# Performance work log

Measured on AMD Instinct MI355X. Metric: run time of the kernel, lower is better.

## Reference

```python
import jax, jax.numpy as jnp
import numpy as np

N, E, D, H = 50000, 800000, 64, 64  # nodes, edges, feat dim, hidden dim
EPS = 1e-3  # Keras BatchNormalization default epsilon

def bn(x, g, b, mu, v):
    # inference-mode batch norm with moving statistics
    return (x - mu) * jax.lax.rsqrt(v + EPS) * g + b

def gelu(x):
    return jax.nn.gelu(x, approximate=False)  # tf.nn.gelu default is exact

def setup_inputs() -> dict:
    key = jax.random.key(0)
    ks = jax.random.split(key, 24)
    r = lambda i, shape, s=1.0: (jax.random.normal(ks[i], shape, jnp.float32) * s)
    inp = {
        "node_feats": r(0, (N, D)),
        "edge_feats": r(1, (E, D)),
        "src": jax.random.randint(ks[2], (E,), 0, N, jnp.int32),
        "dst": jax.random.randint(ks[3], (E,), 0, N, jnp.int32),
        # message MLP (BN -> Dense(gelu)) x2, input D
        "m_g1": 1.0 + 0.1 * r(4, (D,)), "m_b1": 0.1 * r(5, (D,)),
        "m_mu1": 0.1 * r(6, (D,)), "m_v1": jnp.ones((D,), jnp.float32),
        "m_W1": r(7, (D, H), 1.0 / np.sqrt(D)), "m_c1": jnp.zeros((H,), jnp.float32),
        "m_g2": 1.0 + 0.1 * r(8, (H,)), "m_b2": 0.1 * r(9, (H,)),
        "m_mu2": 0.1 * r(10, (H,)), "m_v2": jnp.ones((H,), jnp.float32),
        "m_W2": r(11, (H, H), 1.0 / np.sqrt(H)), "m_c2": jnp.zeros((H,), jnp.float32),
        # edge transformer MLP (Dense(gelu)) x2, input D
        "e_W1": r(12, (D, H), 1.0 / np.sqrt(D)), "e_c1": jnp.zeros((H,), jnp.float32),
        "e_W2": r(13, (H, H), 1.0 / np.sqrt(H)), "e_c2": jnp.zeros((H,), jnp.float32),
        # update MLP (BN -> Dense(gelu)) x2, input D+H (concat combination)
        "u_g1": 1.0 + 0.1 * r(14, (D + H,)), "u_b1": 0.1 * r(15, (D + H,)),
        "u_mu1": 0.1 * r(16, (D + H,)), "u_v1": jnp.ones((D + H,), jnp.float32),
        "u_W1": r(17, (D + H, H), 1.0 / np.sqrt(D + H)), "u_c1": jnp.zeros((H,), jnp.float32),
        "u_g2": 1.0 + 0.1 * r(18, (H,)), "u_b2": 0.1 * r(19, (H,)),
        "u_mu2": 0.1 * r(20, (H,)), "u_v2": jnp.ones((H,), jnp.float32),
        "u_W2": r(21, (H, H), 1.0 / np.sqrt(H)), "u_c2": jnp.zeros((H,), jnp.float32),
    }
    return inp

def reference(node_feats, edge_feats,
              m_g1, m_b1, m_mu1, m_v1, m_W1, m_c1,
              m_g2, m_b2, m_mu2, m_v2, m_W2, m_c2,
              e_W1, e_c1, e_W2, e_c2,
              u_g1, u_b1, u_mu1, u_v1, u_W1, u_c1,
              u_g2, u_b2, u_mu2, u_v2, u_W2, u_c2,
              src, dst):
    # gather neighbour representations: [E, D]
    nbr = node_feats[dst]
    # base message MLP: (BN -> Dropout(identity at inference) -> Dense gelu) x2
    h = gelu(bn(nbr, m_g1, m_b1, m_mu1, m_v1) @ m_W1 + m_c1)
    msg = gelu(bn(h, m_g2, m_b2, m_mu2, m_v2) @ m_W2 + m_c2)
    # edge transformer: Dense(gelu) x2, gates the messages elementwise
    er = gelu(edge_feats @ e_W1 + e_c1)
    er = gelu(er @ e_W2 + e_c2)
    msg = msg * er  # [E, H]
    # unsorted_segment_mean over source node indices (empty segments -> 0)
    s = jax.ops.segment_sum(msg, src, num_segments=N)
    cnt = jax.ops.segment_sum(jnp.ones((E, 1), msg.dtype), src, num_segments=N)
    agg = s / jnp.maximum(cnt, 1.0)  # [N, H]
    # combine ('concat') and update MLP
    hcat = jnp.concatenate([node_feats, agg], axis=-1)  # [N, D+H]
    h = gelu(bn(hcat, u_g1, u_b1, u_mu1, u_v1) @ u_W1 + u_c1)
    out = gelu(bn(h, u_g2, u_b2, u_mu2, u_v2) @ u_W2 + u_c2)
    return out  # [N, H]
```

## Files before the change

kernel.cpp:

```cpp
#include <hip/hip_runtime.h>
#include <hip/hip_bf16.h>

#define NN 50000
#define NE 800000

typedef __bf16 bf16_t;
typedef bf16_t bf16x8 __attribute__((ext_vector_type(8)));
typedef float f32x4 __attribute__((ext_vector_type(4)));

__device__ __forceinline__ float gelu_f(float x) {
    float v = x * fmaf(x * x, 0.07135481627f, 1.595769122f);
    float e = __expf(-v);
    return x * __builtin_amdgcn_rcpf(1.0f + e);
}

__device__ void fold_frag(int K, const float* W, const float* g, const float* b,
                          const float* mu, const float* v, const float* c,
                          bf16_t* Wf, float* cb, int tid, float* part) {
    const int n = tid & 63, kc = tid >> 6;
    const int nt = n >> 4, lrow = n & 15, nkc = K >> 5;
    const int kq = K >> 2, k0 = kc * kq, k1 = k0 + kq;
    float acc = 0.f;
    for (int k = k0; k < k1; ++k) {
        float w = W[k * 64 + n];
        float s = 1.0f, o = 0.0f;
        if (g) {
            s = g[k] * __frsqrt_rn(v[k] + 1e-3f);
            o = b[k] - mu[k] * s;
        }
        int idx = ((nt * nkc + (k >> 5)) * 64 + ((k >> 3) & 3) * 16 + lrow) * 8 + (k & 7);
        Wf[idx] = (bf16_t)(w * s);
        acc += o * w;
    }
    part[kc * 64 + n] = acc;
    __syncthreads();
    if (kc == 0) cb[n] = c[n] + part[n] + part[64 + n] + part[128 + n] + part[192 + n];
}

__global__ void fold_kernel(
    const float* mg1, const float* mb1, const float* mmu1, const float* mv1,
    const float* mW1, const float* mc1,
    const float* mg2, const float* mb2, const float* mmu2, const float* mv2,
    const float* mW2, const float* mc2,
    const float* eW1, const float* ec1, const float* eW2, const float* ec2,
    const float* ug1, const float* ub1, const float* umu1, const float* uv1,
    const float* uW1, const float* uc1,
    const float* ug2, const float* ub2, const float* umu2, const float* uv2,
    const float* uW2, const float* uc2,
    bf16_t* wcat, bf16_t* uW1f, bf16_t* uW2f,
    float* cm1, float* cm2, float* ce1, float* ce2, float* cu1, float* cu2)
{
    __shared__ float part[256];
    int t = threadIdx.x;
    switch (blockIdx.x) {
        case 0: fold_frag(64,  mW1, mg1, mb1, mmu1, mv1, mc1, wcat,         cm1, t, part); break;
        case 1: fold_frag(64,  mW2, mg2, mb2, mmu2, mv2, mc2, wcat + 4096,  cm2, t, part); break;
        case 2: fold_frag(64,  eW1, nullptr, nullptr, nullptr, nullptr, ec1, wcat + 8192,  ce1, t, part); break;
        case 3: fold_frag(64,  eW2, nullptr, nullptr, nullptr, nullptr, ec2, wcat + 12288, ce2, t, part); break;
        case 4: fold_frag(128, uW1, ug1, ub1, umu1, uv1, uc1, uW1f, cu1, t, part); break;
        case 5: fold_frag(64,  uW2, ug2, ub2, umu2, uv2, uc2, uW2f, cu2, t, part); break;
    }
}

__global__ void hist_kernel(const int* __restrict__ src, int* __restrict__ cnt) {
    int e = blockIdx.x * 256 + threadIdx.x;
    if (e < NE) atomicAdd(&cnt[src[e]], 1);
}

__global__ void scanA_kernel(const int* __restrict__ cnt, int* __restrict__ part,
                             int* __restrict__ btot) {
    __shared__ int s[256];
    int tid = threadIdx.x;
    int i = blockIdx.x * 256 + tid;
    int v = (i < NN) ? cnt[i] : 0;
    s[tid] = v;
    __syncthreads();
    #pragma unroll
    for (int off = 1; off < 256; off <<= 1) {
        int t = (tid >= off) ? s[tid - off] : 0;
        __syncthreads();
        s[tid] += t;
        __syncthreads();
    }
    if (i < NN) part[i] = s[tid] - v;
    if (tid == 255) btot[blockIdx.x] = s[255];
}

__global__ void scanB_kernel(int* __restrict__ btot, int nblk) {
    __shared__ int s[256];
    int tid = threadIdx.x;
    int v = (tid < nblk) ? btot[tid] : 0;
    s[tid] = v;
    __syncthreads();
    #pragma unroll
    for (int off = 1; off < 256; off <<= 1) {
        int t = (tid >= off) ? s[tid - off] : 0;
        __syncthreads();
        s[tid] += t;
        __syncthreads();
    }
    if (tid < nblk) btot[tid] = s[tid] - v;
}

__global__ void scanC_kernel(const int* __restrict__ part, const int* __restrict__ btot,
                             int* __restrict__ woff) {
    int i = blockIdx.x * 256 + threadIdx.x;
    if (i < NN) woff[i] = part[i] + btot[i >> 8];
}

__device__ __forceinline__ void mk_frag_hilo(const float* row, int quad,
        bf16x8& hi0, bf16x8& lo0, bf16x8& hi1, bf16x8& lo1)
{
    #pragma unroll
    for (int j = 0; j < 8; ++j) {
        float x0 = row[quad * 8 + j];
        float x1 = row[32 + quad * 8 + j];
        bf16_t h0 = (bf16_t)x0, h1 = (bf16_t)x1;
        hi0[j] = h0; lo0[j] = (bf16_t)(x0 - (float)h0);
        hi1[j] = h1; lo1[j] = (bf16_t)(x1 - (float)h1);
    }
}

__device__ __forceinline__ bf16x8 ldb(const bf16_t* wf, int slot, int lane) {
    return *(const bf16x8*)(wf + (slot * 64 + lane) * 8);
}

__device__ __forceinline__ void gemm64_hilo(const bf16_t* wf, int m,
        bf16x8 h0, bf16x8 l0, bf16x8 h1, bf16x8 l1, f32x4 (&acc)[4], int lane)
{
    #pragma unroll
    for (int nt = 0; nt < 4; ++nt) {
        bf16x8 b0 = ldb(wf, m * 8 + nt * 2 + 0, lane);
        bf16x8 b1 = ldb(wf, m * 8 + nt * 2 + 1, lane);
        f32x4 c = {0.f, 0.f, 0.f, 0.f};
        c = __builtin_amdgcn_mfma_f32_16x16x32_bf16(h0, b0, c, 0, 0, 0);
        c = __builtin_amdgcn_mfma_f32_16x16x32_bf16(l0, b0, c, 0, 0, 0);
        c = __builtin_amdgcn_mfma_f32_16x16x32_bf16(h1, b1, c, 0, 0, 0);
        c = __builtin_amdgcn_mfma_f32_16x16x32_bf16(l1, b1, c, 0, 0, 0);
        acc[nt] = c;
    }
}

__device__ __forceinline__ void gemm64(const bf16_t* wf, int m,
        bf16x8 a0, bf16x8 a1, f32x4 (&acc)[4], int lane)
{
    #pragma unroll
    for (int nt = 0; nt < 4; ++nt) {
        bf16x8 b0 = ldb(wf, m * 8 + nt * 2 + 0, lane);
        bf16x8 b1 = ldb(wf, m * 8 + nt * 2 + 1, lane);
        f32x4 c = {0.f, 0.f, 0.f, 0.f};
        c = __builtin_amdgcn_mfma_f32_16x16x32_bf16(a0, b0, c, 0, 0, 0);
        c = __builtin_amdgcn_mfma_f32_16x16x32_bf16(a1, b1, c, 0, 0, 0);
        acc[nt] = c;
    }
}

__device__ __forceinline__ void epi_to_frag(const f32x4 (&acc)[4], const float* bias,
        bf16_t* h, int lrow, int quad)
{
    #pragma unroll
    for (int nt = 0; nt < 4; ++nt) {
        float bb = bias[nt * 16 + lrow];
        #pragma unroll
        for (int r = 0; r < 4; ++r)
            h[((nt * 2 + (lrow >> 3)) * 16 + quad * 4 + r) * 8 + (lrow & 7)] =
                (bf16_t)gelu_f(acc[nt][r] + bb);
    }
}

__global__ __launch_bounds__(256) void node_msg_kernel(
    const float* __restrict__ node_feats, const bf16_t* __restrict__ wcat,
    const float* __restrict__ cm1, const float* __restrict__ cm2,
    bf16_t* __restrict__ msg)
{
    __shared__ bf16_t wf[8192];
    __shared__ bf16_t hf[4][1024];

    const int tid  = threadIdx.x;
    const int wave = tid >> 6;
    const int lane = tid & 63;
    const int quad = lane >> 4;
    const int lrow = lane & 15;

    #pragma unroll
    for (int i = 0; i < 4; ++i) {
        int chunk = tid + i * 256;
        *(bf16x8*)(wf + chunk * 8) = *(const bf16x8*)(wcat + chunk * 8);
    }
    __syncthreads();

    const int nbase = blockIdx.x * 64 + wave * 16;
    int arow = nbase + lrow;
    arow = arow < NN ? arow : NN - 1;

    f32x4 acc[4];
    {
        const float* nrow = node_feats + (size_t)arow * 64;
        bf16x8 h0, l0, h1, l1;
        mk_frag_hilo(nrow, quad, h0, l0, h1, l1);
        gemm64_hilo(wf, 0, h0, l0, h1, l1, acc, lane);
        epi_to_frag(acc, cm1, hf[wave], lrow, quad);
    }
    bf16x8 a0 = *(const bf16x8*)(hf[wave] + lane * 8);
    bf16x8 a1 = *(const bf16x8*)(hf[wave] + (lane + 64) * 8);
    gemm64(wf, 1, a0, a1, acc, lane);

    #pragma unroll
    for (int nt = 0; nt < 4; ++nt) {
        float bb = cm2[nt * 16 + lrow];
        #pragma unroll
        for (int r = 0; r < 4; ++r) {
            int row = nbase + quad * 4 + r;
            if (row < NN)
                msg[(size_t)row * 64 + nt * 16 + lrow] = (bf16_t)gelu_f(acc[nt][r] + bb);
        }
    }
}

__global__ __launch_bounds__(256) void edge_kernel(
    const float* __restrict__ edge_feats,
    const int* __restrict__ src, const int* __restrict__ dst,
    const bf16_t* __restrict__ wcat,
    const float* __restrict__ ce1, const float* __restrict__ ce2,
    const bf16_t* __restrict__ msg,
    float* __restrict__ s_acc, int* __restrict__ woff,
    bf16_t* __restrict__ buf, int use_csr)
{
    __shared__ bf16_t wf[8192];
    __shared__ bf16_t hf[4][1024];

    const int tid  = threadIdx.x;
    const int wave = tid >> 6;
    const int lane = tid & 63;
    const int quad = lane >> 4;
    const int lrow = lane & 15;

    #pragma unroll
    for (int i = 0; i < 4; ++i) {
        int chunk = tid + i * 256;
        *(bf16x8*)(wf + chunk * 8) = *(const bf16x8*)(wcat + 8192 + chunk * 8);
    }
    __syncthreads();

    const int ebase = blockIdx.x * 64 + wave * 16;
    bf16_t* h = hf[wave];
    const int r0 = lane >> 3;
    const int c0 = lane & 7;
    const int r1 = 8 + r0;
    const int b0 = r0 * 64 + ((c0 * 8) ^ (((r0 >> 2) & 3) << 4));
    const int b1 = r1 * 64 + ((c0 * 8) ^ (((r1 >> 2) & 3) << 4));

    int dA = dst[ebase + r0];
    int dB = dst[ebase + r1];
    bf16x8 mA = *(const bf16x8*)(msg + (size_t)dA * 64 + c0 * 8);
    bf16x8 mB = *(const bf16x8*)(msg + (size_t)dB * 64 + c0 * 8);
    int pe_l = 0;
    if (use_csr && lane < 16) pe_l = atomicAdd(&woff[src[ebase + lane]], 1);

    f32x4 acc[4];
    {
        const float* efr = edge_feats + (size_t)(ebase + lrow) * 64;
        bf16x8 h0_, l0_, h1_, l1_;
        mk_frag_hilo(efr, quad, h0_, l0_, h1_, l1_);
        gemm64_hilo(wf, 0, h0_, l0_, h1_, l1_, acc, lane);
        epi_to_frag(acc, ce1, h, lrow, quad);
    }
    bf16x8 a0 = *(const bf16x8*)(h + lane * 8);
    bf16x8 a1 = *(const bf16x8*)(h + (lane + 64) * 8);
    __builtin_amdgcn_wave_barrier();
    *(bf16x8*)(h + b0) = mA;
    *(bf16x8*)(h + b1) = mB;
    __builtin_amdgcn_wave_barrier();

    gemm64(wf, 1, a0, a1, acc, lane);
    __builtin_amdgcn_wave_barrier();

    if (use_csr) {
        #pragma unroll
        for (int nt = 0; nt < 4; ++nt) {
            float bb = ce2[nt * 16 + lrow];
            #pragma unroll
            for (int r = 0; r < 4; ++r) {
                int e = quad * 4 + r;
                int ci = e * 64 + ((nt * 16 + lrow) ^ (((e >> 2) & 3) << 4));
                float er = gelu_f(acc[nt][r] + bb);
                h[ci] = (bf16_t)(er * (float)h[ci]);
            }
        }
        __builtin_amdgcn_wave_barrier();
        int peA = __shfl(pe_l, r0);
        int peB = __shfl(pe_l, r1);
        bf16x8 gA = *(const bf16x8*)(h + b0);
        bf16x8 gB = *(const bf16x8*)(h + b1);
        *(bf16x8*)(buf + (size_t)peA * 64 + c0 * 8) = gA;
        *(bf16x8*)(buf + (size_t)peB * 64 + c0 * 8) = gB;
    } else {
        #pragma unroll
        for (int nt = 0; nt < 4; ++nt) {
            float bb = ce2[nt * 16 + lrow];
            #pragma unroll
            for (int r = 0; r < 4; ++r) {
                int e = quad * 4 + r;
                int ci = e * 64 + ((nt * 16 + lrow) ^ (((e >> 2) & 3) << 4));
                float er = gelu_f(acc[nt][r] + bb);
                unsafeAtomicAdd(&s_acc[(size_t)src[ebase + e] * 64 + nt * 16 + lrow],
                                er * (float)h[ci]);
            }
        }
    }
}

__global__ __launch_bounds__(256) void agg_kernel(
    const bf16_t* __restrict__ buf, const int* __restrict__ woff,
    const int* __restrict__ cnt, float* __restrict__ agg)
{
    const int wave = threadIdx.x >> 6;
    const int lane = threadIdx.x & 63;
    const int n = blockIdx.x * 4 + wave;
    const int deg = cnt[n];
    const int end = woff[n];
    const int start = end - deg;
    const int rg = lane >> 3;
    const int cc = lane & 7;

    float a[8] = {0.f, 0.f, 0.f, 0.f, 0.f, 0.f, 0.f, 0.f};
    for (int b = start; b < end; b += 8) {
        int row = b + rg;
        if (row < end) {
            bf16x8 v = *(const bf16x8*)(buf + (size_t)row * 64 + cc * 8);
            #pragma unroll
            for (int j = 0; j < 8; ++j) a[j] += (float)v[j];
        }
    }
    #pragma unroll
    for (int off = 8; off < 64; off <<= 1) {
        #pragma unroll
        for (int j = 0; j < 8; ++j) a[j] += __shfl_xor(a[j], off);
    }
    if (lane < 8) {
        float invd = (deg > 0) ? __builtin_amdgcn_rcpf((float)deg) : 0.f;
        float* dstp = agg + (size_t)n * 64 + cc * 8;
        #pragma unroll
        for (int j = 0; j < 8; ++j) dstp[j] = a[j] * invd;
    }
}

__global__ __launch_bounds__(256) void update_kernel(
    const float* __restrict__ node_feats,
    const float* __restrict__ aggv, const int* __restrict__ cnt,
    const bf16_t* __restrict__ uW1f, const float* __restrict__ cu1,
    const bf16_t* __restrict__ uW2f, const float* __restrict__ cu2,
    float* __restrict__ out)
{
    __shared__ bf16_t w1f[8192];
    __shared__ bf16_t w2f[4096];
    __shared__ bf16_t hf[4][1024];

    const int tid  = threadIdx.x;
    const int wave = tid >> 6;
    const int lane = tid & 63;
    const int quad = lane >> 4;
    const int lrow = lane & 15;

    #pragma unroll
    for (int i = 0; i < 4; ++i) {
        int chunk = tid + i * 256;
        *(bf16x8*)(w1f + chunk * 8) = *(const bf16x8*)(uW1f + chunk * 8);
    }
    #pragma unroll
    for (int i = 0; i < 2; ++i) {
        int chunk = tid + i * 256;
        *(bf16x8*)(w2f + chunk * 8) = *(const bf16x8*)(uW2f + chunk * 8);
    }
    __syncthreads();

    const int nbase = blockIdx.x * 64 + wave * 16;
    int arow = nbase + lrow;
    arow = arow < NN ? arow : NN - 1;

    const float* nf   = node_feats + (size_t)arow * 64;
    const float* srow = aggv + (size_t)arow * 64;
    float inv = cnt ? 1.0f / fmaxf((float)cnt[arow], 1.0f) : 1.0f;

    bf16x8 ah[4], al[4];
    #pragma unroll
    for (int j = 0; j < 8; ++j) {
        float x0 = nf[quad * 8 + j];
        float x1 = nf[32 + quad * 8 + j];
        float x2 = srow[quad * 8 + j] * inv;
        float x3 = srow[32 + quad * 8 + j] * inv;
        bf16_t h0 = (bf16_t)x0, h1 = (bf16_t)x1, h2 = (bf16_t)x2, h3 = (bf16_t)x3;
        ah[0][j] = h0; al[0][j] = (bf16_t)(x0 - (float)h0);
        ah[1][j] = h1; al[1][j] = (bf16_t)(x1 - (float)h1);
        ah[2][j] = h2; al[2][j] = (bf16_t)(x2 - (float)h2);
        ah[3][j] = h3; al[3][j] = (bf16_t)(x3 - (float)h3);
    }

    f32x4 acc[4];
    #pragma unroll
    for (int nt = 0; nt < 4; ++nt) {
        f32x4 c = {0.f, 0.f, 0.f, 0.f};
        #pragma unroll
        for (int kk = 0; kk < 4; ++kk) {
            bf16x8 b = *(const bf16x8*)(w1f + ((nt * 4 + kk) * 64 + lane) * 8);
            c = __builtin_amdgcn_mfma_f32_16x16x32_bf16(ah[kk], b, c, 0, 0, 0);
            c = __builtin_amdgcn_mfma_f32_16x16x32_bf16(al[kk], b, c, 0, 0, 0);
        }
        acc[nt] = c;
    }
    bf16_t* hb = hf[wave];
    epi_to_frag(acc, cu1, hb, lrow, quad);

    bf16x8 ha0 = *(const bf16x8*)(hb + lane * 8);
    bf16x8 ha1 = *(const bf16x8*)(hb + (lane + 64) * 8);
    gemm64(w2f, 0, ha0, ha1, acc, lane);

    #pragma unroll
    for (int nt = 0; nt < 4; ++nt) {
        int col = nt * 16 + lrow;
        float bb = cu2[col];
        #pragma unroll
        for (int r = 0; r < 4; ++r) {
            int row = nbase + quad * 4 + r;
            if (row < NN)
                out[(size_t)row * 64 + col] = gelu_f(acc[nt][r] + bb);
        }
    }
}

extern "C" void kernel_launch(void* const* d_in, const int* in_sizes, int n_in,
                              void* d_out, int out_size, void* d_ws, size_t ws_size,
                              hipStream_t stream) {
    const float* node_feats = (const float*)d_in[0];
    const float* edge_feats = (const float*)d_in[1];
    const int*   src        = (const int*)d_in[2];
    const int*   dst        = (const int*)d_in[3];

    char* ws = (char*)d_ws;
    const bool csr = ws_size >= (size_t)116500000;

    size_t off = 0;
    bf16_t* buf = nullptr; float* agg = nullptr; bf16_t* msg = nullptr;
    float* s_acc = nullptr; int* cnt = nullptr; int* woff = nullptr;
    int* part = nullptr; int* btot = nullptr;

    if (csr) {
        buf = (bf16_t*)(ws + off); off += (size_t)NE * 128;
        char* aggbase = ws + off;
        agg = (float*)aggbase;     off += (size_t)NN * 256;
        msg = (bf16_t*)(aggbase + (size_t)NE * 4);
        cnt  = (int*)(ws + off); off += (size_t)NN * 4;
        woff = (int*)(ws + off); off += (size_t)NN * 4;
        part = (int*)(ws + off); off += (size_t)NN * 4;
        btot = (int*)(ws + off); off += 1024;
    } else {
        s_acc = (float*)(ws + off);  off += (size_t)NN * 256;
        cnt   = (int*)(ws + off);    off += (size_t)NN * 4;
        msg   = (bf16_t*)(ws + off); off += (size_t)NN * 128;
    }
    bf16_t* wcat = (bf16_t*)(ws + off); off += 32768;
    bf16_t* uW1f = (bf16_t*)(ws + off); off += 16384;
    bf16_t* uW2f = (bf16_t*)(ws + off); off += 8192;
    float* cm1 = (float*)(ws + off); off += 256;
    float* cm2 = (float*)(ws + off); off += 256;
    float* ce1 = (float*)(ws + off); off += 256;
    float* ce2 = (float*)(ws + off); off += 256;
    float* cu1 = (float*)(ws + off); off += 256;
    float* cu2 = (float*)(ws + off); off += 256;

    if (csr) {
        hipMemsetAsync(cnt, 0, (size_t)NN * 4, stream);
    } else {
        hipMemsetAsync(s_acc, 0, (size_t)NN * 256 + (size_t)NN * 4, stream);
    }

    fold_kernel<<<6, 256, 0, stream>>>(
        (const float*)d_in[4],  (const float*)d_in[5],  (const float*)d_in[6],  (const float*)d_in[7],
        (const float*)d_in[8],  (const float*)d_in[9],
        (const float*)d_in[10], (const float*)d_in[11], (const float*)d_in[12], (const float*)d_in[13],
        (const float*)d_in[14], (const float*)d_in[15],
        (const float*)d_in[16], (const float*)d_in[17], (const float*)d_in[18], (const float*)d_in[19],
        (const float*)d_in[20], (const float*)d_in[21], (const float*)d_in[22], (const float*)d_in[23],
        (const float*)d_in[24], (const float*)d_in[25],
        (const float*)d_in[26], (const float*)d_in[27], (const float*)d_in[28], (const float*)d_in[29],
        (const float*)d_in[30], (const float*)d_in[31],
        wcat, uW1f, uW2f, cm1, cm2, ce1, ce2, cu1, cu2);

    node_msg_kernel<<<(NN + 63) / 64, 256, 0, stream>>>(node_feats, wcat, cm1, cm2, msg);

    hist_kernel<<<(NE + 255) / 256, 256, 0, stream>>>(src, cnt);

    if (csr) {
        const int NBLK = (NN + 255) / 256;
        scanA_kernel<<<NBLK, 256, 0, stream>>>(cnt, part, btot);
        scanB_kernel<<<1, 256, 0, stream>>>(btot, NBLK);
        scanC_kernel<<<NBLK, 256, 0, stream>>>(part, btot, woff);
    }

    edge_kernel<<<NE / 64, 256, 0, stream>>>(
        edge_feats, src, dst, wcat, ce1, ce2, msg, s_acc, woff, buf, csr ? 1 : 0);

    if (csr) {
        agg_kernel<<<NN / 4, 256, 0, stream>>>(buf, woff, cnt, agg);
        update_kernel<<<(NN + 63) / 64, 256, 0, stream>>>(
            node_feats, agg, nullptr, uW1f, cu1, uW2f, cu2, (float*)d_out);
    } else {
        update_kernel<<<(NN + 63) / 64, 256, 0, stream>>>(
            node_feats, s_acc, cnt, uW1f, cu1, uW2f, cu2, (float*)d_out);
    }
}
```

Measured before the change: 482.9 us.

## Write edge messages in edge order with index list and fuse aggregation into update

The edge kernel now writes gated messages contiguously by edge id and records each edge's CSR slot in an index array, rather than scattering message rows to their CSR positions. The separate aggregation kernel is removed; the update kernel gathers each node's messages through the index array, averages them into shared memory and feeds them straight to the update MLP. This drops the fp32 agg round trip and one launch, and makes the message stores coalesced. In exchange, aggregation reads become indirect and scattered, and each wave walks 16 nodes serially, so uneven degrees can stall it. The atomic-accumulate fallback for small workspaces is removed, and scan scratch now aliases the message buffer.

Result: slower. 558.7 us (+15.7%).

```diff
diff --git a/kernel.cpp b/kernel.cpp
--- a/kernel.cpp
+++ b/kernel.cpp
@@ -223,8 +223,8 @@
     const bf16_t* __restrict__ wcat,
     const float* __restrict__ ce1, const float* __restrict__ ce2,
     const bf16_t* __restrict__ msg,
-    float* __restrict__ s_acc, int* __restrict__ woff,
-    bf16_t* __restrict__ buf, int use_csr)
+    int* __restrict__ woff, int* __restrict__ eidx,
+    bf16_t* __restrict__ buf)
 {
     __shared__ bf16_t wf[8192];
     __shared__ bf16_t hf[4][1024];
@@ -254,8 +254,10 @@
     int dB = dst[ebase + r1];
     bf16x8 mA = *(const bf16x8*)(msg + (size_t)dA * 64 + c0 * 8);
     bf16x8 mB = *(const bf16x8*)(msg + (size_t)dB * 64 + c0 * 8);
-    int pe_l = 0;
-    if (use_csr && lane < 16) pe_l = atomicAdd(&woff[src[ebase + lane]], 1);
+    if (lane < 16) {
+        int p = atomicAdd(&woff[src[ebase + lane]], 1);
+        eidx[p] = ebase + lane;
+    }
 
     f32x4 acc[4];
     {
@@ -275,79 +277,29 @@
     gemm64(wf, 1, a0, a1, acc, lane);
     __builtin_amdgcn_wave_barrier();
 
-    if (use_csr) {
-        #pragma unroll
-        for (int nt = 0; nt < 4; ++nt) {
-            float bb = ce2[nt * 16 + lrow];
-            #pragma unroll
-            for (int r = 0; r < 4; ++r) {
-                int e = quad * 4 + r;
-                int ci = e * 64 + ((nt * 16 + lrow) ^ (((e >> 2) & 3) << 4));
-                float er = gelu_f(acc[nt][r] + bb);
-                h[ci] = (bf16_t)(er * (float)h[ci]);
-            }
-        }
-        __builtin_amdgcn_wave_barrier();
-        int peA = __shfl(pe_l, r0);
-        int peB = __shfl(pe_l, r1);
-        bf16x8 gA = *(const bf16x8*)(h + b0);
-        bf16x8 gB = *(const bf16x8*)(h + b1);
-        *(bf16x8*)(buf + (size_t)peA * 64 + c0 * 8) = gA;
-        *(bf16x8*)(buf + (size_t)peB * 64 + c0 * 8) = gB;
-    } else {
-        #pragma unroll
-        for (int nt = 0; nt < 4; ++nt) {
-            float bb = ce2[nt * 16 + lrow];
-            #pragma unroll
-            for (int r = 0; r < 4; ++r) {
-                int e = quad * 4 + r;
-                int ci = e * 64 + ((nt * 16 + lrow) ^ (((e >> 2) & 3) << 4));
-                float er = gelu_f(acc[nt][r] + bb);
-                unsafeAtomicAdd(&s_acc[(size_t)src[ebase + e] * 64 + nt * 16 + lrow],
-                                er * (float)h[ci]);
-            }
-        }
-    }
-}
-
-__global__ __launch_bounds__(256) void agg_kernel(
-    const bf16_t* __restrict__ buf, const int* __restrict__ woff,
-    const int* __restrict__ cnt, float* __restrict__ agg)
-{
-    const int wave = threadIdx.x >> 6;
-    const int lane = threadIdx.x & 63;
-    const int n = blockIdx.x * 4 + wave;
-    const int deg = cnt[n];
-    const int end = woff[n];
-    const int start = end - deg;
-    const int rg = lane >> 3;
-    const int cc = lane & 7;
-
-    float a[8] = {0.f, 0.f, 0.f, 0.f, 0.f, 0.f, 0.f, 0.f};
-    for (int b = start; b < end; b += 8) {
-        int row = b + rg;
-        if (row < end) {
-            bf16x8 v = *(const bf16x8*)(buf + (size_t)row * 64 + cc * 8);
-            #pragma unroll
-            for (int j = 0; j < 8; ++j) a[j] += (float)v[j];
-        }
-    }
-    #pragma unroll
-    for (int off = 8; off < 64; off <<= 1) {
-        #pragma unroll
-        for (int j = 0; j < 8; ++j) a[j] += __shfl_xor(a[j], off);
-    }
-    if (lane < 8) {
-        float invd = (deg > 0) ? __builtin_amdgcn_rcpf((float)deg) : 0.f;
-        float* dstp = agg + (size_t)n * 64 + cc * 8;
-        #pragma unroll
-        for (int j = 0; j < 8; ++j) dstp[j] = a[j] * invd;
-    }
+    #pragma unroll
+    for (int nt = 0; nt < 4; ++nt) {
+        float bb = ce2[nt * 16 + lrow];
+        #pragma unroll
+        for (int r = 0; r < 4; ++r) {
+            int e = quad * 4 + r;
+            int ci = e * 64 + ((nt * 16 + lrow) ^ (((e >> 2) & 3) << 4));
+            float er = gelu_f(acc[nt][r] + bb);
+            h[ci] = (bf16_t)(er * (float)h[ci]);
+        }
+    }
+    __builtin_amdgcn_wave_barrier();
+
+    bf16x8 gA = *(const bf16x8*)(h + b0);
+    bf16x8 gB = *(const bf16x8*)(h + b1);
+    *(bf16x8*)(buf + (size_t)(ebase + r0) * 64 + c0 * 8) = gA;
+    *(bf16x8*)(buf + (size_t)(ebase + r1) * 64 + c0 * 8) = gB;
 }
 
 __global__ __launch_bounds__(256) void update_kernel(
     const float* __restrict__ node_feats,
-    const float* __restrict__ aggv, const int* __restrict__ cnt,
+    const bf16_t* __restrict__ buf, const int* __restrict__ eidx,
+    const int* __restrict__ woff, const int* __restrict__ cnt,
     const bf16_t* __restrict__ uW1f, const float* __restrict__ cu1,
     const bf16_t* __restrict__ uW2f, const float* __restrict__ cu2,
     float* __restrict__ out)
@@ -355,6 +307,7 @@
     __shared__ bf16_t w1f[8192];
     __shared__ bf16_t w2f[4096];
     __shared__ bf16_t hf[4][1024];
+    __shared__ float aggl[4][16][68];
 
     const int tid  = threadIdx.x;
     const int wave = tid >> 6;
@@ -375,20 +328,50 @@
     __syncthreads();
 
     const int nbase = blockIdx.x * 64 + wave * 16;
+    const int rg = lane >> 3;
+    const int cc = lane & 7;
+    float* al_ = &aggl[wave][0][0];
+
+    for (int i = 0; i < 16; ++i) {
+        int nn = nbase + i; nn = nn < NN ? nn : NN - 1;
+        int end = woff[nn];
+        int deg = cnt[nn];
+        int start = end - deg;
+        float a[8] = {0.f, 0.f, 0.f, 0.f, 0.f, 0.f, 0.f, 0.f};
+        for (int b = start; b < end; b += 8) {
+            int row = b + rg;
+            if (row < end) {
+                int e = eidx[row];
+                bf16x8 v = *(const bf16x8*)(buf + (size_t)e * 64 + cc * 8);
+                #pragma unroll
+                for (int j = 0; j < 8; ++j) a[j] += (float)v[j];
+            }
+        }
+        #pragma unroll
+        for (int off = 8; off < 64; off <<= 1) {
+            #pragma unroll
+            for (int j = 0; j < 8; ++j) a[j] += __shfl_xor(a[j], off);
+        }
+        if (lane < 8) {
+            float invd = (deg > 0) ? __builtin_amdgcn_rcpf((float)deg) : 0.f;
+            #pragma unroll
+            for (int j = 0; j < 8; ++j) al_[i * 68 + cc * 8 + j] = a[j] * invd;
+        }
+    }
+    __builtin_amdgcn_wave_barrier();
+
     int arow = nbase + lrow;
     arow = arow < NN ? arow : NN - 1;
-
     const float* nf   = node_feats + (size_t)arow * 64;
-    const float* srow = aggv + (size_t)arow * 64;
-    float inv = cnt ? 1.0f / fmaxf((float)cnt[arow], 1.0f) : 1.0f;
+    const float* srow = al_ + lrow * 68;
 
     bf16x8 ah[4], al[4];
     #pragma unroll
     for (int j = 0; j < 8; ++j) {
         float x0 = nf[quad * 8 + j];
         float x1 = nf[32 + quad * 8 + j];
-        float x2 = srow[quad * 8 + j] * inv;
-        float x3 = srow[32 + quad * 8 + j] * inv;
+        float x2 = srow[quad * 8 + j];
+        float x3 = srow[32 + quad * 8 + j];
         bf16_t h0 = (bf16_t)x0, h1 = (bf16_t)x1, h2 = (bf16_t)x2, h3 = (bf16_t)x3;
         ah[0][j] = h0; al[0][j] = (bf16_t)(x0 - (float)h0);
         ah[1][j] = h1; al[1][j] = (bf16_t)(x1 - (float)h1);
@@ -437,27 +420,14 @@
     const int*   dst        = (const int*)d_in[3];
 
     char* ws = (char*)d_ws;
-    const bool csr = ws_size >= (size_t)116500000;
-
     size_t off = 0;
-    bf16_t* buf = nullptr; float* agg = nullptr; bf16_t* msg = nullptr;
-    float* s_acc = nullptr; int* cnt = nullptr; int* woff = nullptr;
-    int* part = nullptr; int* btot = nullptr;
-
-    if (csr) {
-        buf = (bf16_t*)(ws + off); off += (size_t)NE * 128;
-        char* aggbase = ws + off;
-        agg = (float*)aggbase;     off += (size_t)NN * 256;
-        msg = (bf16_t*)(aggbase + (size_t)NE * 4);
-        cnt  = (int*)(ws + off); off += (size_t)NN * 4;
-        woff = (int*)(ws + off); off += (size_t)NN * 4;
-        part = (int*)(ws + off); off += (size_t)NN * 4;
-        btot = (int*)(ws + off); off += 1024;
-    } else {
-        s_acc = (float*)(ws + off);  off += (size_t)NN * 256;
-        cnt   = (int*)(ws + off);    off += (size_t)NN * 4;
-        msg   = (bf16_t*)(ws + off); off += (size_t)NN * 128;
-    }
+    bf16_t* buf  = (bf16_t*)(ws + off); off += (size_t)NE * 128;
+    int*    part = (int*)buf;
+    int*    btot = (int*)(ws) + NN;
+    bf16_t* msg  = (bf16_t*)(ws + off); off += (size_t)NN * 128;
+    int*    eidx = (int*)(ws + off);    off += (size_t)NE * 4;
+    int*    cnt  = (int*)(ws + off);    off += (size_t)NN * 4;
+    int*    woff = (int*)(ws + off);    off += (size_t)NN * 4;
     bf16_t* wcat = (bf16_t*)(ws + off); off += 32768;
     bf16_t* uW1f = (bf16_t*)(ws + off); off += 16384;
     bf16_t* uW2f = (bf16_t*)(ws + off); off += 8192;
@@ -468,11 +438,7 @@
     float* cu1 = (float*)(ws + off); off += 256;
     float* cu2 = (float*)(ws + off); off += 256;
 
-    if (csr) {
-        hipMemsetAsync(cnt, 0, (size_t)NN * 4, stream);
-    } else {
-        hipMemsetAsync(s_acc, 0, (size_t)NN * 256 + (size_t)NN * 4, stream);
-    }
+    hipMemsetAsync(cnt, 0, (size_t)NN * 4, stream);
 
     fold_kernel<<<6, 256, 0, stream>>>(
         (const float*)d_in[4],  (const float*)d_in[5],  (const float*)d_in[6],  (const float*)d_in[7],
@@ -490,22 +456,14 @@
 
     hist_kernel<<<(NE + 255) / 256, 256, 0, stream>>>(src, cnt);
 
-    if (csr) {
-        const int NBLK = (NN + 255) / 256;
-        scanA_kernel<<<NBLK, 256, 0, stream>>>(cnt, part, btot);
-        scanB_kernel<<<1, 256, 0, stream>>>(btot, NBLK);
-        scanC_kernel<<<NBLK, 256, 0, stream>>>(part, btot, woff);
-    }
+    const int NBLK = (NN + 255) / 256;
+    scanA_kernel<<<NBLK, 256, 0, stream>>>(cnt, part, btot);
+    scanB_kernel<<<1, 256, 0, stream>>>(btot, NBLK);
+    scanC_kernel<<<NBLK, 256, 0, stream>>>(part, btot, woff);
 
     edge_kernel<<<NE / 64, 256, 0, stream>>>(
-        edge_feats, src, dst, wcat, ce1, ce2, msg, s_acc, woff, buf, csr ? 1 : 0);
-
-    if (csr) {
-        agg_kernel<<<NN / 4, 256, 0, stream>>>(buf, woff, cnt, agg);
-        update_kernel<<<(NN + 63) / 64, 256, 0, stream>>>(
-            node_feats, agg, nullptr, uW1f, cu1, uW2f, cu2, (float*)d_out);
-    } else {
-        update_kernel<<<(NN + 63) / 64, 256, 0, stream>>>(
-            node_feats, s_acc, cnt, uW1f, cu1, uW2f, cu2, (float*)d_out);
-    }
-}
+        edge_feats, src, dst, wcat, ce1, ce2, msg, woff, eidx, buf);
+
+    update_kernel<<<(NN + 63) / 64, 256, 0, stream>>>(
+        node_feats, buf, eidx, woff, cnt, uW1f, cu1, uW2f, cu2, (float*)d_out);
+}
```
